# Kernel tuning notes

Measured on AMD Instinct MI355X. Metric: run time of the kernel, lower is better.

The kernel has to match this reference:

```python
import jax, jax.numpy as jnp
import numpy as np

B, S, DM, H = 4, 2048, 768, 12
HD = DM // H
HEAD_Z = float(np.sqrt(HD))


def norm_layer(x, scale, bias):
    # custom normalization over last dim: (x - mean)/std * scale + bias, scalar scale/bias, no eps
    mean = x.mean(axis=2, keepdims=True)
    std = jnp.sqrt(((x - mean) ** 2).mean(axis=2, keepdims=True))
    return (x - mean) / std * scale + bias


def setup_inputs() -> dict:
    key = jax.random.key(0)
    ks = jax.random.split(key, 12)
    s = 1.0 / np.sqrt(DM)
    return {
        "base": jax.random.normal(ks[0], (B, S, DM), dtype=jnp.float32),
        "Wqkv": jax.random.normal(ks[1], (DM, 3 * DM), dtype=jnp.float32) * s,
        "bqkv": jax.random.normal(ks[2], (3 * DM,), dtype=jnp.float32) * s,
        "W1": jax.random.normal(ks[3], (DM, DM), dtype=jnp.float32) * s,
        "b1": jax.random.normal(ks[4], (DM,), dtype=jnp.float32) * s,
        "W2": jax.random.normal(ks[5], (DM, DM), dtype=jnp.float32) * s,
        "b2": jax.random.normal(ks[6], (DM,), dtype=jnp.float32) * s,
        "n1_scale": jax.random.uniform(ks[7], (1,), jnp.float32, -s, s) + 0.5,
        "n1_bias": jax.random.uniform(ks[8], (1,), jnp.float32, -s, s),
        "n2_scale": jax.random.uniform(ks[9], (1,), jnp.float32, -s, s) + 0.5,
        "n2_bias": jax.random.uniform(ks[10], (1,), jnp.float32, -s, s),
    }


def reference(base, Wqkv, bqkv, W1, b1, W2, b2, n1_scale, n1_bias, n2_scale, n2_bias):
    qkv = base @ Wqkv + bqkv                     # [B,S,3*DM]
    q, k, v = jnp.split(qkv, 3, axis=2)
    # per-head attention, vectorized over heads: the torch loop with broadcast-mul-sum
    # is mathematically softmax(QK^T/sqrt(hd)) @ V per head
    q = q.reshape(B, S, H, HD)
    k = k.reshape(B, S, H, HD)
    v = v.reshape(B, S, H, HD)
    scores = jnp.einsum('bqhd,bkhd->bhqk', q, k) / HEAD_Z  # [B,H,S,S]
    attn = jax.nn.softmax(scores, axis=-1)
    av = jnp.einsum('bhqk,bkhd->bqhd', attn, v).reshape(B, S, DM)
    hidden = norm_layer(av @ W1 + b1 + base, n1_scale, n1_bias)
    out = norm_layer(jax.nn.relu(hidden @ W2 + b2) + hidden, n2_scale, n2_bias)
    return out
```

## Files before the change

kernel.cpp:

```cpp
#include <hip/hip_runtime.h>
#include <hip/hip_bf16.h>
#include <stdint.h>

#define B_ 4
#define S_ 2048
#define DM_ 768
#define H_ 12
#define HD_ 64
#define ROWS (B_*S_)
#define QKVN (3*DM_)

typedef __attribute__((ext_vector_type(8))) short short8;
typedef __attribute__((ext_vector_type(4))) float floatx4;
typedef __attribute__((ext_vector_type(8))) unsigned short ushort8;
typedef __attribute__((ext_vector_type(4))) unsigned short ushort4v;
typedef __attribute__((ext_vector_type(4))) float float4_t;

__device__ __forceinline__ unsigned short f2b(float f) {
  union { float f; uint32_t u; } x; x.f = f;
  uint32_t r = x.u + 0x7FFFu + ((x.u >> 16) & 1u);
  return (unsigned short)(r >> 16);
}
__device__ __forceinline__ float b2f(unsigned short u) {
  union { uint32_t u; float f; } x; x.u = ((uint32_t)u) << 16; return x.f;
}
__device__ __forceinline__ uint32_t fbits(float f) {
  union { float f; uint32_t u; } x; x.f = f; return x.u;
}

__device__ __forceinline__ void load_lds16(const void* g, void* l) {
  __builtin_amdgcn_global_load_lds(
      (const __attribute__((address_space(1))) uint32_t*)g,
      (__attribute__((address_space(3))) uint32_t*)l, 16, 0, 0);
}

#define CVT_B 6144
#define WQ_B 1728
#define W1_B 576
__global__ __launch_bounds__(256) void prep(
    const float* __restrict__ base, unsigned short* __restrict__ base_bf,
    const float* __restrict__ Wqkv, unsigned short* __restrict__ Wqkvt,
    const float* __restrict__ W1, unsigned short* __restrict__ W1t,
    const float* __restrict__ W2, unsigned short* __restrict__ W2t) {
  __shared__ float t[32][33];
  int bid = blockIdx.x;
  int tid = threadIdx.x;
  if (bid < CVT_B) {
    int i = bid * 256 + tid;
    float4_t v = ((const float4_t*)base)[i];
    ushort4v o;
    o[0] = f2b(v[0]); o[1] = f2b(v[1]); o[2] = f2b(v[2]); o[3] = f2b(v[3]);
    ((ushort4v*)base_bf)[i] = o;
    return;
  }
  const float* W; unsigned short* Wt; int N, rel;
  if (bid < CVT_B + WQ_B)      { W = Wqkv; Wt = Wqkvt; N = QKVN; rel = bid - CVT_B; }
  else if (bid < CVT_B + WQ_B + W1_B) { W = W1; Wt = W1t; N = DM_; rel = bid - CVT_B - WQ_B; }
  else                          { W = W2; Wt = W2t; N = DM_; rel = bid - CVT_B - WQ_B - W1_B; }
  int K = DM_;
  int n0 = (rel % (N / 32)) * 32, k0 = (rel / (N / 32)) * 32;
  int tx = tid & 31, ty = tid >> 5;
#pragma unroll
  for (int i = 0; i < 4; i++)
    t[ty + i * 8][tx] = W[(size_t)(k0 + ty + i * 8) * N + n0 + tx];
  __syncthreads();
#pragma unroll
  for (int i = 0; i < 4; i++)
    Wt[(size_t)(n0 + ty + i * 8) * K + k0 + tx] = f2b(t[tx][ty + i * 8]);
}

__global__ __launch_bounds__(256, 2) void gemm_qkv(
    const unsigned short* __restrict__ A,
    const unsigned short* __restrict__ Bt,
    const float* __restrict__ bias,
    unsigned short* __restrict__ Cout,
    unsigned short* __restrict__ Vt,
    int M, int N, int K) {
  __shared__ __align__(16) unsigned short LDSbuf[2 * 128 * 128];
  unsigned short* As = LDSbuf;
  unsigned short* Bs = LDSbuf + 128 * 128;
  int tid = threadIdx.x;
  int wave = tid >> 6, lane = tid & 63;
  int quad = lane >> 4, l16 = lane & 15;
  int sr4 = lane >> 4;
  int c16 = lane & 15;
  int flat = blockIdx.x;
  int xcd = flat & 7, widx = flat >> 3;
  int mb = xcd * 8 + (widx & 7);
  int nb = widx >> 3;
  int m0 = mb * 128, n0 = nb * 128;
  int wm = (wave >> 1) * 64, wn = (wave & 1) * 64;
  floatx4 acc[4][4] = {};

  for (int kb = 0; kb < K; kb += 128) {
#pragma unroll
    for (int i = 0; i < 8; i++) {
      int op = wave * 8 + i;
      int srow = op * 4 + sr4;
      int sc = c16 ^ (srow & 15);
      load_lds16(A + (size_t)(m0 + srow) * K + kb + sc * 8, (char*)As + op * 1024);
    }
#pragma unroll
    for (int i = 0; i < 8; i++) {
      int op = wave * 8 + i;
      int srow = op * 4 + sr4;
      int sc = c16 ^ (srow & 15);
      load_lds16(Bt + (size_t)(n0 + srow) * K + kb + sc * 8, (char*)Bs + op * 1024);
    }
    __syncthreads();
#pragma unroll
    for (int ks = 0; ks < 4; ks++) {
      short8 af[4], bfr[4];
#pragma unroll
      for (int mt = 0; mt < 4; mt++)
        af[mt] = *(const short8*)(As + (wm + mt * 16 + l16) * 128 + ((ks * 4 + quad) ^ l16) * 8);
#pragma unroll
      for (int nt = 0; nt < 4; nt++)
        bfr[nt] = *(const short8*)(Bs + (wn + nt * 16 + l16) * 128 + ((ks * 4 + quad) ^ l16) * 8);
#pragma unroll
      for (int mt = 0; mt < 4; mt++)
#pragma unroll
        for (int nt = 0; nt < 4; nt++)
          acc[mt][nt] = __builtin_amdgcn_mfma_f32_16x16x32_bf16(af[mt], bfr[nt], acc[mt][nt], 0, 0, 0);
    }
    __syncthreads();
  }

  if (n0 < 2 * DM_) {
#pragma unroll
    for (int mt = 0; mt < 4; mt++) {
#pragma unroll
      for (int nt = 0; nt < 4; nt++) {
#pragma unroll
        for (int r = 0; r < 4; r++) {
          int row = m0 + wm + mt * 16 + quad * 4 + r;
          int col = n0 + wn + nt * 16 + l16;
          float v = acc[mt][nt][r] + bias[col];
          if (col < DM_) v *= 0.18033688011112042f;
          Cout[(size_t)row * N + col] = f2b(v);
        }
      }
    }
  } else {
    unsigned short* scr = LDSbuf + wave * 4608;
    int h = (n0 + wn - 2 * DM_) >> 6;
    int b = m0 >> 11;
    int s_base = (m0 & (S_ - 1)) + wm;
#pragma unroll
    for (int nt = 0; nt < 4; nt++) {
      float bv = bias[n0 + wn + nt * 16 + l16];
      ushort8 v0, v1;
#pragma unroll
      for (int j = 0; j < 8; j++) {
        v0[j] = f2b(acc[j & 3][nt][j >> 2] + bv);
        v1[j] = f2b(acc[j & 3][nt][2 + (j >> 2)] + bv);
      }
      *(ushort8*)(scr + (nt * 16 + l16) * 72 + quad * 16) = v0;
      *(ushort8*)(scr + (nt * 16 + l16) * 72 + quad * 16 + 8) = v1;
    }
#pragma unroll
    for (int it = 0; it < 8; it++) {
      int d = it * 8 + (lane >> 3);
      int ch = lane & 7;
      ushort8 w = *(const ushort8*)(scr + d * 72 + ch * 8);
      *(ushort8*)(Vt + ((size_t)(b * H_ + h) * 64 + d) * S_ + s_base + ch * 8) = w;
    }
  }
}

template <int EPI>
__global__ __launch_bounds__(256, 4) void gemm64(
    const unsigned short* __restrict__ A,
    const unsigned short* __restrict__ Bt,
    const float* __restrict__ bias,
    const unsigned short* __restrict__ res,
    unsigned short* __restrict__ Cout,
    int M, int N, int K) {
  __shared__ __align__(16) unsigned short As[64 * 64];
  __shared__ __align__(16) unsigned short Bs[128 * 64];
  int tid = threadIdx.x;
  int wave = tid >> 6, lane = tid & 63;
  int quad = lane >> 4, l16 = lane & 15;
  int e = l16 & 7;
  int sr = lane >> 3;
  int sc = (lane & 7) ^ (sr & 7);
  int flat = blockIdx.x;
  int xcd = flat & 7, widx = flat >> 3;
  int mb = xcd * 16 + (widx & 15);
  int nb = widx >> 4;
  int m0 = mb * 64, n0 = nb * 128;
  int wm = (wave >> 1) * 32, wn = (wave & 1) * 64;
  floatx4 acc[2][4] = {};

  for (int kb = 0; kb < K; kb += 64) {
#pragma unroll
    for (int i = 0; i < 2; i++) {
      int op = wave * 2 + i;
      load_lds16(A + (size_t)(m0 + op * 8 + sr) * K + kb + sc * 8, (char*)As + op * 1024);
    }
#pragma unroll
    for (int i = 0; i < 4; i++) {
      int op = wave * 4 + i;
      load_lds16(Bt + (size_t)(n0 + op * 8 + sr) * K + kb + sc * 8, (char*)Bs + op * 1024);
    }
    __syncthreads();
#pragma unroll
    for (int ks = 0; ks < 2; ks++) {
      short8 af[2], bfr[4];
#pragma unroll
      for (int mt = 0; mt < 2; mt++)
        af[mt] = *(const short8*)(As + (wm + mt * 16 + l16) * 64 + ((ks * 4 + quad) ^ e) * 8);
#pragma unroll
      for (int nt = 0; nt < 4; nt++)
        bfr[nt] = *(const short8*)(Bs + (wn + nt * 16 + l16) * 64 + ((ks * 4 + quad) ^ e) * 8);
#pragma unroll
      for (int mt = 0; mt < 2; mt++)
#pragma unroll
        for (int nt = 0; nt < 4; nt++)
          acc[mt][nt] = __builtin_amdgcn_mfma_f32_16x16x32_bf16(af[mt], bfr[nt], acc[mt][nt], 0, 0, 0);
    }
    __syncthreads();
  }
#pragma unroll
  for (int mt = 0; mt < 2; mt++) {
#pragma unroll
    for (int nt = 0; nt < 4; nt++) {
#pragma unroll
      for (int r = 0; r < 4; r++) {
        int row = m0 + wm + mt * 16 + quad * 4 + r;
        int col = n0 + wn + nt * 16 + l16;
        size_t idx = (size_t)row * N + col;
        float v = acc[mt][nt][r] + bias[col];
        if (EPI == 2) v = fmaxf(v, 0.0f);
        v += b2f(res[idx]);
        Cout[idx] = f2b(v);
      }
    }
  }
}

__global__ __launch_bounds__(256, 3) void attn(
    const unsigned short* __restrict__ qkv,
    const unsigned short* __restrict__ Vt,
    unsigned short* __restrict__ av) {
  int flat = blockIdx.x;
  int widx = (flat & 7) * 96 + (flat >> 3);
  int qt = widx & 15;
  int bh = widx >> 4;
  int b = bh / H_, h = bh % H_;
  int row0 = b * S_ + qt * 128;
  __shared__ __align__(16) unsigned short Ks[2][64 * 64];
  __shared__ __align__(16) unsigned short Vs[2][64 * 64];
  __shared__ __align__(16) unsigned short Ps[4][32 * 72];
  int tid = threadIdx.x;
  int wave = tid >> 6, lane = tid & 63;
  int quad = lane >> 4, l16 = lane & 15;
  int e = l16 & 7;
  int sr = lane >> 3;
  int sc = (lane & 7) ^ (sr & 7);

#pragma unroll
  for (int i = 0; i < 4; i++) {
    load_lds16(qkv + (size_t)(row0 + wave * 32 + i * 8 + sr) * QKVN + h * HD_ + sc * 8,
               (char*)Ps[wave] + i * 1024);
  }
  const unsigned short* kp = qkv + (size_t)(b * S_ + wave * 16 + sr) * QKVN + DM_ + h * HD_ + sc * 8;
  const unsigned short* vp = Vt + ((size_t)bh * 64 + wave * 16 + sr) * S_ + sc * 8;
  auto stageKV = [&](const unsigned short* kq, const unsigned short* vq, int buf) {
#pragma unroll
    for (int i = 0; i < 2; i++) {
      load_lds16(kq + (size_t)i * 8 * QKVN, (char*)Ks[buf] + wave * 2048 + i * 1024);
      load_lds16(vq + (size_t)i * 8 * S_, (char*)Vs[buf] + wave * 2048 + i * 1024);
    }
  };
  stageKV(kp, vp, 0);

  floatx4 accO[2][4] = {};
  floatx4 accL[2] = {};
  short8 ones;
#pragma unroll
  for (int j = 0; j < 8; j++) ones[j] = (short)0x3F80;
  __syncthreads();

  short8 qf[2][2];
#pragma unroll
  for (int mf = 0; mf < 2; mf++)
#pragma unroll
    for (int ks = 0; ks < 2; ks++)
      qf[mf][ks] = *(const short8*)(Ps[wave] + (mf * 16 + l16) * 64 + ((ks * 4 + quad) ^ e) * 8);

  int cur = 0;
  for (int kt = 0; kt < 32; kt++) {
    if (kt + 1 < 32) {
      kp += 64 * QKVN;
      vp += 64;
      stageKV(kp, vp, cur ^ 1);
    }
    floatx4 sv[2][4] = {};
    __builtin_amdgcn_s_setprio(1);
#pragma unroll
    for (int ks = 0; ks < 2; ks++)
#pragma unroll
      for (int nt = 0; nt < 4; nt++) {
        short8 kf = *(const short8*)(Ks[cur] + (nt * 16 + l16) * 64 + ((ks * 4 + quad) ^ e) * 8);
#pragma unroll
        for (int mf = 0; mf < 2; mf++)
          sv[mf][nt] = __builtin_amdgcn_mfma_f32_16x16x32_bf16(qf[mf][ks], kf, sv[mf][nt], 0, 0, 0);
      }
    __builtin_amdgcn_s_setprio(0);
#pragma unroll
    for (int mf = 0; mf < 2; mf++)
#pragma unroll
      for (int r = 0; r < 4; r++) {
        uint32_t u0 = fbits(__builtin_amdgcn_exp2f(sv[mf][0][r]));
        uint32_t u1 = fbits(__builtin_amdgcn_exp2f(sv[mf][1][r]));
        uint32_t u2 = fbits(__builtin_amdgcn_exp2f(sv[mf][2][r]));
        uint32_t u3 = fbits(__builtin_amdgcn_exp2f(sv[mf][3][r]));
        uint2 val;
        val.x = __builtin_amdgcn_perm(u1, u0, 0x07060302u);
        val.y = __builtin_amdgcn_perm(u3, u2, 0x07060302u);
        *(uint2*)(&Ps[wave][(mf * 16 + quad * 4 + r) * 72 + l16 * 4]) = val;
      }
    __builtin_amdgcn_s_setprio(1);
#pragma unroll
    for (int ks = 0; ks < 2; ks++) {
      short8 pf[2];
#pragma unroll
      for (int mf = 0; mf < 2; mf++) {
        pf[mf] = *(const short8*)(Ps[wave] + (mf * 16 + l16) * 72 + ks * 32 + quad * 8);
        accL[mf] = __builtin_amdgcn_mfma_f32_16x16x32_bf16(pf[mf], ones, accL[mf], 0, 0, 0);
      }
#pragma unroll
      for (int nt = 0; nt < 4; nt++) {
        short8 vf = *(const short8*)(Vs[cur] + (nt * 16 + l16) * 64 + ((ks * 4 + quad) ^ e) * 8);
#pragma unroll
        for (int mf = 0; mf < 2; mf++)
          accO[mf][nt] = __builtin_amdgcn_mfma_f32_16x16x32_bf16(pf[mf], vf, accO[mf][nt], 0, 0, 0);
      }
    }
    __builtin_amdgcn_s_setprio(0);
    __syncthreads();
    cur ^= 1;
  }
#pragma unroll
  for (int mf = 0; mf < 2; mf++)
#pragma unroll
    for (int r = 0; r < 4; r++) {
      float inv = 1.0f / accL[mf][r];
      int row = row0 + wave * 32 + mf * 16 + quad * 4 + r;
#pragma unroll
      for (int nt = 0; nt < 4; nt++)
        av[(size_t)row * DM_ + h * HD_ + nt * 16 + l16] = f2b(accO[mf][nt][r] * inv);
    }
}

template <int WB>
__global__ __launch_bounds__(256) void normk(
    const unsigned short* __restrict__ X, const float* __restrict__ scale,
    const float* __restrict__ bias, float* __restrict__ Y,
    unsigned short* __restrict__ Ybf) {
  int row = blockIdx.x;
  const unsigned short* x = X + (size_t)row * DM_;
  int tid = threadIdx.x;
  int wave = tid >> 6, lane = tid & 63;
  float v[3];
#pragma unroll
  for (int i = 0; i < 3; i++) v[i] = b2f(x[tid + i * 256]);
  float s = v[0] + v[1] + v[2];
#pragma unroll
  for (int o = 32; o > 0; o >>= 1) s += __shfl_xor(s, o);
  __shared__ float red[4];
  if (lane == 0) red[wave] = s;
  __syncthreads();
  float mean = (red[0] + red[1] + red[2] + red[3]) * (1.0f / DM_);
  float ss = 0.0f;
#pragma unroll
  for (int i = 0; i < 3; i++) { v[i] -= mean; ss += v[i] * v[i]; }
#pragma unroll
  for (int o = 32; o > 0; o >>= 1) ss += __shfl_xor(ss, o);
  __syncthreads();
  if (lane == 0) red[wave] = ss;
  __syncthreads();
  float var = (red[0] + red[1] + red[2] + red[3]) * (1.0f / DM_);
  float rstd = rsqrtf(var);
  float sg = scale[0], bg = bias[0];
#pragma unroll
  for (int i = 0; i < 3; i++) {
    float y = v[i] * rstd * sg + bg;
    if (WB) Ybf[(size_t)row * DM_ + tid + i * 256] = f2b(y);
    else    Y[(size_t)row * DM_ + tid + i * 256] = y;
  }
}

extern "C" void kernel_launch(void* const* d_in, const int* in_sizes, int n_in,
                              void* d_out, int out_size, void* d_ws, size_t ws_size,
                              hipStream_t stream) {
  const float* base = (const float*)d_in[0];
  const float* Wqkv = (const float*)d_in[1];
  const float* bqkv = (const float*)d_in[2];
  const float* W1 = (const float*)d_in[3];
  const float* b1 = (const float*)d_in[4];
  const float* W2 = (const float*)d_in[5];
  const float* b2 = (const float*)d_in[6];
  const float* n1s = (const float*)d_in[7];
  const float* n1b = (const float*)d_in[8];
  const float* n2s = (const float*)d_in[9];
  const float* n2b = (const float*)d_in[10];
  float* out = (float*)d_out;

  char* ws = (char*)d_ws;
  size_t off = 0;
  auto alloc = [&](size_t bytes) {
    char* p = ws + off;
    off = (off + bytes + 255) & ~(size_t)255;
    return p;
  };
  unsigned short* base_bf = (unsigned short*)alloc((size_t)ROWS * DM_ * 2);
  unsigned short* Wqkvt = (unsigned short*)alloc((size_t)QKVN * DM_ * 2);
  unsigned short* W1t = (unsigned short*)alloc((size_t)DM_ * DM_ * 2);
  unsigned short* W2t = (unsigned short*)alloc((size_t)DM_ * DM_ * 2);
  unsigned short* qkvb = (unsigned short*)alloc((size_t)ROWS * QKVN * 2);
  unsigned short* Vtb = (unsigned short*)alloc((size_t)B_ * H_ * HD_ * S_ * 2);
  unsigned short* avb = (unsigned short*)alloc((size_t)ROWS * DM_ * 2);
  unsigned short* t1b = (unsigned short*)alloc((size_t)ROWS * DM_ * 2);
  unsigned short* hbf = (unsigned short*)alloc((size_t)ROWS * DM_ * 2);

  prep<<<CVT_B + WQ_B + 2 * W1_B, 256, 0, stream>>>(
      base, base_bf, Wqkv, Wqkvt, W1, W1t, W2, W2t);
  gemm_qkv<<<dim3((QKVN / 128) * (ROWS / 128)), 256, 0, stream>>>(
      base_bf, Wqkvt, bqkv, qkvb, Vtb, ROWS, QKVN, DM_);
  attn<<<dim3((S_ / 128) * (B_ * H_)), 256, 0, stream>>>(qkvb, Vtb, avb);
  gemm64<1><<<dim3((DM_ / 128) * (ROWS / 64)), 256, 0, stream>>>(
      avb, W1t, b1, base_bf, t1b, ROWS, DM_, DM_);
  normk<1><<<ROWS, 256, 0, stream>>>(t1b, n1s, n1b, nullptr, hbf);
  gemm64<2><<<dim3((DM_ / 128) * (ROWS / 64)), 256, 0, stream>>>(
      hbf, W2t, b2, hbf, t1b, ROWS, DM_, DM_);
  normk<0><<<ROWS, 256, 0, stream>>>(t1b, n2s, n2b, out, nullptr);
}
```

Baseline: 246.8 us.

## Fold first normalization into GEMM epilogues via row-stat atomics and algebraic rewrite

```diff
diff --git a/kernel.cpp b/kernel.cpp
--- a/kernel.cpp
+++ b/kernel.cpp
@@ -37,11 +37,13 @@
 #define CVT_B 6144
 #define WQ_B 1728
 #define W1_B 576
+#define PREP_B (CVT_B + WQ_B + 2 * W1_B + 64 + 3)
 __global__ __launch_bounds__(256) void prep(
     const float* __restrict__ base, unsigned short* __restrict__ base_bf,
     const float* __restrict__ Wqkv, unsigned short* __restrict__ Wqkvt,
     const float* __restrict__ W1, unsigned short* __restrict__ W1t,
-    const float* __restrict__ W2, unsigned short* __restrict__ W2t) {
+    const float* __restrict__ W2, unsigned short* __restrict__ W2t,
+    float* __restrict__ rs1, float* __restrict__ rq1, float* __restrict__ cs2) {
   __shared__ float t[32][33];
   int bid = blockIdx.x;
   int tid = threadIdx.x;
@@ -51,6 +53,19 @@
     ushort4v o;
     o[0] = f2b(v[0]); o[1] = f2b(v[1]); o[2] = f2b(v[2]); o[3] = f2b(v[3]);
     ((ushort4v*)base_bf)[i] = o;
+    return;
+  }
+  if (bid >= CVT_B + WQ_B + 2 * W1_B) {
+    int r2 = bid - (CVT_B + WQ_B + 2 * W1_B);
+    if (r2 < 64) {
+      int i = r2 * 256 + tid;
+      if (i < ROWS) rs1[i] = 0.0f; else rq1[i - ROWS] = 0.0f;
+      return;
+    }
+    int col = (r2 - 64) * 256 + tid;
+    float s = 0.0f;
+    for (int k = 0; k < DM_; k++) s += W2[(size_t)k * DM_ + col];
+    cs2[col] = s;
     return;
   }
   const float* W; unsigned short* Wt; int N, rel;
@@ -126,23 +141,26 @@
     __syncthreads();
   }
 
+  unsigned short* scr = LDSbuf + wave * 4608;
   if (n0 < 2 * DM_) {
-#pragma unroll
-    for (int mt = 0; mt < 4; mt++) {
-#pragma unroll
-      for (int nt = 0; nt < 4; nt++) {
-#pragma unroll
-        for (int r = 0; r < 4; r++) {
-          int row = m0 + wm + mt * 16 + quad * 4 + r;
-          int col = n0 + wn + nt * 16 + l16;
-          float v = acc[mt][nt][r] + bias[col];
-          if (col < DM_) v *= 0.18033688011112042f;
-          Cout[(size_t)row * N + col] = f2b(v);
-        }
-      }
+    float qs = (n0 < DM_) ? 0.18033688011112042f : 1.0f;
+#pragma unroll
+    for (int nt = 0; nt < 4; nt++) {
+      float bv = bias[n0 + wn + nt * 16 + l16];
+#pragma unroll
+      for (int mt = 0; mt < 4; mt++)
+#pragma unroll
+        for (int r = 0; r < 4; r++)
+          scr[(mt * 16 + quad * 4 + r) * 72 + nt * 16 + l16] = f2b((acc[mt][nt][r] + bv) * qs);
+    }
+#pragma unroll
+    for (int it = 0; it < 8; it++) {
+      int row = it * 8 + (lane >> 3);
+      int ch = lane & 7;
+      ushort8 w = *(const ushort8*)(scr + row * 72 + ch * 8);
+      *(ushort8*)(Cout + (size_t)(m0 + wm + row) * N + n0 + wn + ch * 8) = w;
     }
   } else {
-    unsigned short* scr = LDSbuf + wave * 4608;
     int h = (n0 + wn - 2 * DM_) >> 6;
     int b = m0 >> 11;
     int s_base = (m0 & (S_ - 1)) + wm;
@@ -175,6 +193,9 @@
     const float* __restrict__ bias,
     const unsigned short* __restrict__ res,
     unsigned short* __restrict__ Cout,
+    float* __restrict__ rs, float* __restrict__ rq,
+    const float* __restrict__ cs2,
+    const float* __restrict__ nsc, const float* __restrict__ nbi,
     int M, int N, int K) {
   __shared__ __align__(16) unsigned short As[64 * 64];
   __shared__ __align__(16) unsigned short Bs[128 * 64];
@@ -221,19 +242,54 @@
     }
     __syncthreads();
   }
-#pragma unroll
-  for (int mt = 0; mt < 2; mt++) {
-#pragma unroll
-    for (int nt = 0; nt < 4; nt++) {
+  const float inv768 = 1.0f / (float)DM_;
+  if (EPI == 1) {
+#pragma unroll
+    for (int mt = 0; mt < 2; mt++) {
+#pragma unroll
+      for (int r = 0; r < 4; r++) {
+        float srow = 0.0f, qrow = 0.0f;
+        int row = m0 + wm + mt * 16 + quad * 4 + r;
+#pragma unroll
+        for (int nt = 0; nt < 4; nt++) {
+          int col = n0 + wn + nt * 16 + l16;
+          size_t idx = (size_t)row * N + col;
+          float v = acc[mt][nt][r] + bias[col] + b2f(res[idx]);
+          unsigned short vb = f2b(v);
+          Cout[idx] = vb;
+          float vr = b2f(vb);
+          srow += vr; qrow += vr * vr;
+        }
+#pragma unroll
+        for (int o = 1; o < 16; o <<= 1) {
+          srow += __shfl_xor(srow, o);
+          qrow += __shfl_xor(qrow, o);
+        }
+        if (l16 == 0) {
+          atomicAdd(&rs[row], srow);
+          atomicAdd(&rq[row], qrow);
+        }
+      }
+    }
+  } else {
+    float sg = nsc[0], bg = nbi[0];
+#pragma unroll
+    for (int mt = 0; mt < 2; mt++) {
 #pragma unroll
       for (int r = 0; r < 4; r++) {
         int row = m0 + wm + mt * 16 + quad * 4 + r;
-        int col = n0 + wn + nt * 16 + l16;
-        size_t idx = (size_t)row * N + col;
-        float v = acc[mt][nt][r] + bias[col];
-        if (EPI == 2) v = fmaxf(v, 0.0f);
-        v += b2f(res[idx]);
-        Cout[idx] = f2b(v);
+        float mean = rs[row] * inv768;
+        float a = rsqrtf(rq[row] * inv768 - mean * mean) * sg;
+        float c = bg - mean * a;
+#pragma unroll
+        for (int nt = 0; nt < 4; nt++) {
+          int col = n0 + wn + nt * 16 + l16;
+          size_t idx = (size_t)row * N + col;
+          float g = a * acc[mt][nt][r] + c * cs2[col] + bias[col];
+          g = fmaxf(g, 0.0f);
+          float hid = a * b2f(res[idx]) + c;
+          Cout[idx] = f2b(g + hid);
+        }
       }
     }
   }
@@ -424,16 +480,18 @@
   unsigned short* avb = (unsigned short*)alloc((size_t)ROWS * DM_ * 2);
   unsigned short* t1b = (unsigned short*)alloc((size_t)ROWS * DM_ * 2);
   unsigned short* hbf = (unsigned short*)alloc((size_t)ROWS * DM_ * 2);
-
-  prep<<<CVT_B + WQ_B + 2 * W1_B, 256, 0, stream>>>(
-      base, base_bf, Wqkv, Wqkvt, W1, W1t, W2, W2t);
+  float* rs1 = (float*)alloc((size_t)ROWS * 4);
+  float* rq1 = (float*)alloc((size_t)ROWS * 4);
+  float* cs2 = (float*)alloc((size_t)DM_ * 4);
+
+  prep<<<PREP_B, 256, 0, stream>>>(
+      base, base_bf, Wqkv, Wqkvt, W1, W1t, W2, W2t, rs1, rq1, cs2);
   gemm_qkv<<<dim3((QKVN / 128) * (ROWS / 128)), 256, 0, stream>>>(
       base_bf, Wqkvt, bqkv, qkvb, Vtb, ROWS, QKVN, DM_);
   attn<<<dim3((S_ / 128) * (B_ * H_)), 256, 0, stream>>>(qkvb, Vtb, avb);
   gemm64<1><<<dim3((DM_ / 128) * (ROWS / 64)), 256, 0, stream>>>(
-      avb, W1t, b1, base_bf, t1b, ROWS, DM_, DM_);
-  normk<1><<<ROWS, 256, 0, stream>>>(t1b, n1s, n1b, nullptr, hbf);
+      avb, W1t, b1, base_bf, t1b, rs1, rq1, nullptr, nullptr, nullptr, ROWS, DM_, DM_);
   gemm64<2><<<dim3((DM_ / 128) * (ROWS / 64)), 256, 0, stream>>>(
-      hbf, W2t, b2, hbf, t1b, ROWS, DM_, DM_);
-  normk<0><<<ROWS, 256, 0, stream>>>(t1b, n2s, n2b, out, nullptr);
-}
+      t1b, W2t, b2, t1b, hbf, rs1, rq1, cs2, n1s, n1b, ROWS, DM_, DM_);
+  normk<0><<<ROWS, 256, 0, stream>>>(hbf, n2s, n2b, out, nullptr);
+}
```

Measured after the change: 277.7 us. 12.5% more time.
